# Kernel optimization log

Hardware: AMD Instinct MI355X
Metric: run time of the kernel (lower is better)

## Reference

```python
import jax, jax.numpy as jnp
import numpy as np
import math

EPS = 1e-5

def _ln(x, g, b):
    m = jnp.mean(x, axis=-1, keepdims=True)
    v = jnp.var(x, axis=-1, keepdims=True)
    return (x - m) * jax.lax.rsqrt(v + EPS) * g + b

def _rn_layer(x, W, g, b, A, Bb, Rw):
    # x: (B,S,in) -> (B,S,out). W: (out,in), A: (out,basis), Bb: (basis,out)
    S = x.shape[1]
    basis_dim = Bb.shape[0]
    n = _ln(x @ W.T, g, b)                      # (B,S,out)
    j = jnp.arange(S) % basis_dim               # (S,)
    Bv = Bb[j]                                  # (S,out)
    scal = jnp.einsum('bsd,sd->bs', n, Bv)      # (B,S)
    Av = A[:, j].T                              # (S,out)
    nf = scal[..., None] * Av                   # (B,S,out)
    res = x if Rw is None else x @ Rw.T
    return nf + res

def _ts_layer(x, M, g, b, P, Rw):
    # x: (B,S,in) -> (B,S,out). M: (out,in), P: (out,out,G)
    S = x.shape[1]
    D, _, G = P.shape
    t = _ln(x @ M.T, g, b)                      # (B,S,out)
    k = jnp.arange(S, dtype=jnp.float32)
    periods = (jnp.arange(D, dtype=jnp.float32)[:, None, None] * (D * G)
               + jnp.arange(D, dtype=jnp.float32)[None, :, None] * G
               + jnp.arange(G, dtype=jnp.float32)[None, None, :] + 2.0)  # (D,D,G)
    phi = jnp.cos(2.0 * math.pi * k[:, None, None, None] / periods)       # (S,D,D,G)
    # Nk[b,s,i] = sum_{j,g} P[i,j,g] * t[b,s,j] * phi[s,i,j,g]
    Wp = jnp.einsum('ijg,sijg->sij', P, phi)    # (S,D,D)
    Nk = jnp.einsum('sij,bsj->bsi', Wp, t)      # (B,S,D)
    return Nk + x @ Rw.T

def setup_inputs() -> dict:
    key = jax.random.key(0)
    ks = jax.random.split(key, 16)
    B, S = 2, 2048
    d0, d1, d2 = 512, 64, 512        # input_dim, ts out, final out
    bas1, G, bas3 = 64, 8, 64
    u = lambda k, sh, a: jax.random.uniform(k, sh, jnp.float32, -a, a)
    inp = {
        'x':  jax.random.normal(ks[0], (B, S, d0), jnp.float32),
        # Layer 1: RN 512->512 (in==out -> no residual proj)
        'W1': u(ks[1], (d0, d0), 0.1),
        'g1': jnp.ones((d0,), jnp.float32),
        'b1': jnp.zeros((d0,), jnp.float32),
        'A1': u(ks[2], (d0, bas1), 0.1),
        'B1': u(ks[3], (bas1, d0), 0.1),
        # Layer 2: TS 512->64
        'M2': u(ks[4], (d1, d0), 0.5),
        'g2': jnp.ones((d1,), jnp.float32),
        'b2': jnp.zeros((d1,), jnp.float32),
        'P2': u(ks[5], (d1, d1, G), 0.1),
        'R2': u(ks[6], (d1, d0), 0.1),
        # Layer 3: RN 64->512
        'W3': u(ks[7], (d2, d1), 0.1),
        'g3': jnp.ones((d2,), jnp.float32),
        'b3': jnp.zeros((d2,), jnp.float32),
        'A3': u(ks[8], (d2, bas3), 0.1),
        'B3': u(ks[9], (bas3, d2), 0.1),
        'R3': u(ks[10], (d2, d1), 0.1),
    }
    return inp

def reference(x, W1, g1, b1, A1, B1, M2, g2, b2, P2, R2, W3, g3, b3, A3, B3, R3):
    h = _rn_layer(x, W1, g1, b1, A1, B1, None)   # (B,S,512), identity residual
    h = _ts_layer(h, M2, g2, b2, P2, R2)         # (B,S,64)
    h = _rn_layer(h, W3, g3, b3, A3, B3, R3)     # (B,S,512)
    return h
```

## Files before the change

### kernel.cpp

```cpp
#include <hip/hip_runtime.h>
#include <math.h>

#define SEQ  2048
#define ROWS 4096
#define D0   512
#define D1   64
#define C2S  524288

typedef short bf8 __attribute__((ext_vector_type(8)));
typedef float f4  __attribute__((ext_vector_type(4)));

__device__ __forceinline__ unsigned short f2bf(float f) {
    unsigned u = __float_as_uint(f);
    return (unsigned short)((u + 0x7fffu + ((u >> 16) & 1u)) >> 16);
}
__device__ __forceinline__ float bf2f(unsigned short u) {
    return __uint_as_float((unsigned)u << 16);
}
__device__ __forceinline__ void hilo(float f, unsigned short& h, unsigned short& l) {
    h = f2bf(f);
    float fh = bf2f(h);
    l = f2bf(f - fh);
}
__device__ __forceinline__ void cv4h(unsigned short* dh, int idx, float4 v) {
    ushort4 hv;
    hv.x = f2bf(v.x); hv.y = f2bf(v.y); hv.z = f2bf(v.z); hv.w = f2bf(v.w);
    *(ushort4*)(dh + idx) = hv;
}

__device__ __forceinline__ void async16(const void* g, void* l) {
    __builtin_amdgcn_global_load_lds(
        (const __attribute__((address_space(1))) unsigned int*)g,
        (__attribute__((address_space(3))) unsigned int*)l, 16, 0, 0);
}

__global__ __launch_bounds__(256) void convk(
        const float* __restrict__ x,  const float* __restrict__ W1,
        const float* __restrict__ M2, const float* __restrict__ R2,
        const float* __restrict__ W3, const float* __restrict__ R3,
        const float* __restrict__ A1, const float* __restrict__ A3,
        unsigned short* __restrict__ xh, unsigned short* __restrict__ xl,
        unsigned short* __restrict__ W1h,
        unsigned short* __restrict__ C2h,
        unsigned short* __restrict__ C3h,
        float* __restrict__ A3T,
        float* __restrict__ G2y, float* __restrict__ G2r) {
    __shared__ float sh[4][64];
    int c = blockIdx.x, tid = threadIdx.x;
    if (c < 1024) {
        int base = c * 2048 + tid * 4;
        float4 v0 = *(const float4*)(x + base);
        float4 v1 = *(const float4*)(x + base + 1024);
        ushort4 h, l;
        hilo(v0.x, h.x, l.x); hilo(v0.y, h.y, l.y);
        hilo(v0.z, h.z, l.z); hilo(v0.w, h.w, l.w);
        *(ushort4*)(xh + base) = h; *(ushort4*)(xl + base) = l;
        hilo(v1.x, h.x, l.x); hilo(v1.y, h.y, l.y);
        hilo(v1.z, h.z, l.z); hilo(v1.w, h.w, l.w);
        *(ushort4*)(xh + base + 1024) = h; *(ushort4*)(xl + base + 1024) = l;
    } else if (c < 1216) {
        const float* src; unsigned short* dh; int off;
        if      (c < 1152) { src = W1; dh = W1h;         off = c - 1024; }
        else if (c < 1168) { src = M2; dh = C2h;         off = c - 1152; }
        else if (c < 1184) { src = R2; dh = C2h + 32768; off = c - 1168; }
        else if (c < 1200) { src = W3; dh = C3h;         off = c - 1184; }
        else               { src = R3; dh = C3h + 32768; off = c - 1200; }
        int base = off * 2048 + tid * 4;
        cv4h(dh, base,        *(const float4*)(src + base));
        cv4h(dh, base + 1024, *(const float4*)(src + base + 1024));
    } else if (c < 1344) {
        int gid = (c - 1216) * 256 + tid;
        int i = gid >> 6, j = gid & 63;
        A3T[j * 512 + i] = A3[gid];
    } else {
        int jrow = (c - 1344) & 63;
        const float* wv = (c < 1408) ? (M2 + jrow * 512) : (R2 + jrow * 512);
        float* G = (c < 1408) ? G2y : G2r;
        int jm = tid & 63, q = tid >> 6;
        const float* ap = A1 + (q * 128) * 64 + jm;
        const float* wp = wv + q * 128;
        float acc = 0.f;
        for (int cc = 0; cc < 128; ++cc)
            acc = fmaf(ap[cc * 64], wp[cc], acc);
        sh[q][jm] = acc;
        __syncthreads();
        if (tid < 64)
            G[tid * 64 + jrow] = (sh[0][tid] + sh[1][tid]) + (sh[2][tid] + sh[3][tid]);
    }
}

template<int AMODE, int OM>
__global__ __launch_bounds__(256, 4) void gemm128t(
        const unsigned short* __restrict__ Ah, const unsigned short* __restrict__ Al,
        const unsigned short* __restrict__ Wh,
        float* __restrict__ Cf, unsigned short* __restrict__ Cb,
        int N, int K, int Ks) {
    __shared__ __align__(16) unsigned short aH[8192];
    __shared__ __align__(16) unsigned short aL[AMODE ? 8192 : 16];
    __shared__ __align__(16) unsigned short wHs[4096];
    const int tid = threadIdx.x;
    const int wv  = tid >> 6;
    const int ln  = tid & 63;
    const int lm  = ln & 15;
    const int lq  = ln >> 4;
    const int bm  = blockIdx.y * 128;
    const int bn  = blockIdx.x * 64;
    const int k0  = blockIdx.z * Ks;
    const bool alo = (AMODE == 1) || (AMODE == 2 && bn >= 512);

    f4 acc[2][4] = {};

    for (int kt = 0; kt < Ks; kt += 64) {
        const int kg = k0 + kt;
        __syncthreads();
#pragma unroll
        for (int i = 0; i < 4; ++i) {
            int slot = i * 256 + wv * 64 + ln;
            int row  = slot >> 3;
            int ch   = (slot & 7) ^ (row & 7);
            size_t go = (size_t)(bm + row) * K + kg + ch * 8;
            async16(Ah + go, aH + slot * 8);
            if (alo) async16(Al + go, aL + slot * 8);
        }
#pragma unroll
        for (int i = 0; i < 2; ++i) {
            int slot = i * 256 + wv * 64 + ln;
            int row  = slot >> 3;
            int ch   = (slot & 7) ^ (row & 7);
            size_t go = (size_t)(bn + row) * K + kg + ch * 8;
            async16(Wh + go, wHs + slot * 8);
        }
        __syncthreads();

#pragma unroll
        for (int kk = 0; kk < 2; ++kk) {
            const int ck = kk * 4 + lq;
            bf8 a_h[2], a_l[2], b_h[4];
#pragma unroll
            for (int t = 0; t < 2; ++t) {
                int r = wv * 32 + t * 16 + lm;
                a_h[t] = *(const bf8*)(aH + r * 64 + ((ck ^ (r & 7)) * 8));
                if (alo)
                    a_l[t] = *(const bf8*)(aL + r * 64 + ((ck ^ (r & 7)) * 8));
            }
#pragma unroll
            for (int u = 0; u < 4; ++u) {
                int rb = u * 16 + lm;
                b_h[u] = *(const bf8*)(wHs + rb * 64 + ((ck ^ (rb & 7)) * 8));
            }
#pragma unroll
            for (int t = 0; t < 2; ++t)
#pragma unroll
                for (int u = 0; u < 4; ++u) {
                    acc[t][u] = __builtin_amdgcn_mfma_f32_16x16x32_bf16(a_h[t], b_h[u], acc[t][u], 0, 0, 0);
                    if (alo)
                        acc[t][u] = __builtin_amdgcn_mfma_f32_16x16x32_bf16(a_l[t], b_h[u], acc[t][u], 0, 0, 0);
                }
        }
    }

#pragma unroll
    for (int t = 0; t < 2; ++t)
#pragma unroll
        for (int u = 0; u < 4; ++u) {
            int row = bm + wv * 32 + t * 16 + lq * 4;
            int col = bn + u * 16 + lm;
#pragma unroll
            for (int r = 0; r < 4; ++r) {
                float v = acc[t][u][r];
                if constexpr (OM == 2) {
                    if (col < 512) Cb[(size_t)(row + r) * 512 + col] = f2bf(v);
                    else           Cf[(size_t)(row + r) * 512 + col - 512] = v;
                } else {
                    if (col < 512)
                        Cb[(size_t)blockIdx.z * ROWS * 512 + (size_t)(row + r) * 512 + col] = f2bf(v);
                    else
                        Cf[(size_t)blockIdx.z * ROWS * 128 + (size_t)(row + r) * 128 + (col - 512)] = v;
                }
            }
        }
}

__global__ __launch_bounds__(256) void ptk(
        const unsigned short* __restrict__ C1b,
        const float* __restrict__ C2,
        const float* __restrict__ B1,
        const float* __restrict__ g1, const float* __restrict__ b1,
        const float* __restrict__ g2, const float* __restrict__ b2,
        const float* __restrict__ G2y, const float* __restrict__ G2r,
        float* __restrict__ t, float* __restrict__ rsum) {
    const int row = blockIdx.x * 4 + (threadIdx.x >> 6);
    const int l = threadIdx.x & 63;
    const int c = l * 8;
    const int jm = row & 63;
    const size_t rb0 = (size_t)row * 512 + c;
    ushort4 ua = *(const ushort4*)(C1b + rb0);
    ushort4 ub = *(const ushort4*)(C1b + rb0 + 4);
    ushort4 va = *(const ushort4*)(C1b + (size_t)ROWS * 512 + rb0);
    ushort4 vb = *(const ushort4*)(C1b + (size_t)ROWS * 512 + rb0 + 4);
    float y[8];
    y[0] = bf2f(ua.x) + bf2f(va.x); y[1] = bf2f(ua.y) + bf2f(va.y);
    y[2] = bf2f(ua.z) + bf2f(va.z); y[3] = bf2f(ua.w) + bf2f(va.w);
    y[4] = bf2f(ub.x) + bf2f(vb.x); y[5] = bf2f(ub.y) + bf2f(vb.y);
    y[6] = bf2f(ub.z) + bf2f(vb.z); y[7] = bf2f(ub.w) + bf2f(vb.w);
    float4 B0  = *(const float4*)(B1 + jm * 512 + c);
    float4 B1q = *(const float4*)(B1 + jm * 512 + c + 4);
    float4 gg0 = *(const float4*)(g1 + c), gg1 = *(const float4*)(g1 + c + 4);
    float4 bb0 = *(const float4*)(b1 + c), bb1 = *(const float4*)(b1 + c + 4);
    float Bv[8] = {B0.x, B0.y, B0.z, B0.w, B1q.x, B1q.y, B1q.z, B1q.w};
    float gv[8] = {gg0.x, gg0.y, gg0.z, gg0.w, gg1.x, gg1.y, gg1.z, gg1.w};
    float bv[8] = {bb0.x, bb0.y, bb0.z, bb0.w, bb1.x, bb1.y, bb1.z, bb1.w};
    float sum = 0.f, ssq = 0.f, S1 = 0.f, SU = 0.f, SBB = 0.f;
#pragma unroll
    for (int i = 0; i < 8; ++i) {
        float u = gv[i] * Bv[i];
        sum += y[i];
        ssq = fmaf(y[i], y[i], ssq);
        S1  = fmaf(y[i], u, S1);
        SU  += u;
        SBB = fmaf(bv[i], Bv[i], SBB);
    }
#pragma unroll
    for (int m = 1; m < 64; m <<= 1) {
        sum += __shfl_xor(sum, m, 64);
        ssq += __shfl_xor(ssq, m, 64);
        S1  += __shfl_xor(S1, m, 64);
        SU  += __shfl_xor(SU, m, 64);
        SBB += __shfl_xor(SBB, m, 64);
    }
    float mean = sum * (1.0f / 512.0f);
    float var  = ssq * (1.0f / 512.0f) - mean * mean;
    float rstd = rsqrtf(var + 1e-5f);
    float p = rstd * (S1 - mean * SU) + SBB;

    const size_t rb = (size_t)row * 128;
    float z  = C2[rb + l]      + C2[C2S + rb + l];
    float zr = C2[rb + 64 + l] + C2[C2S + rb + 64 + l];
    float v  = z  + p * G2y[jm * 64 + l];
    float rv = zr + p * G2r[jm * 64 + l];
    float s2 = v, q2 = v * v;
#pragma unroll
    for (int m = 1; m < 64; m <<= 1) {
        s2 += __shfl_xor(s2, m, 64);
        q2 += __shfl_xor(q2, m, 64);
    }
    float mean2 = s2 * (1.0f / 64.0f);
    float var2  = q2 * (1.0f / 64.0f) - mean2 * mean2;
    float rstd2 = rsqrtf(var2 + 1e-5f);
    t[row * 64 + l]    = (v - mean2) * rstd2 * g2[l] + b2[l];
    rsum[row * 64 + l] = rv;
}

__global__ __launch_bounds__(256) void lnrn(
        const unsigned short* __restrict__ Yb0,
        const float* __restrict__ RES,
        const float* __restrict__ g, const float* __restrict__ be,
        const float* __restrict__ Bb, const float* __restrict__ AaT,
        float* __restrict__ outf) {
    const int row = blockIdx.x * 4 + (threadIdx.x >> 6);
    const int l = threadIdx.x & 63;
    const int c = l * 8;
    ushort4 ua = *(const ushort4*)(Yb0 + (size_t)row * D0 + c);
    ushort4 ub = *(const ushort4*)(Yb0 + (size_t)row * D0 + c + 4);
    float4 y0, y1;
    y0.x = bf2f(ua.x); y0.y = bf2f(ua.y); y0.z = bf2f(ua.z); y0.w = bf2f(ua.w);
    y1.x = bf2f(ub.x); y1.y = bf2f(ub.y); y1.z = bf2f(ub.z); y1.w = bf2f(ub.w);
    float sum = y0.x + y0.y + y0.z + y0.w + y1.x + y1.y + y1.z + y1.w;
    float ssq = y0.x*y0.x + y0.y*y0.y + y0.z*y0.z + y0.w*y0.w
              + y1.x*y1.x + y1.y*y1.y + y1.z*y1.z + y1.w*y1.w;
#pragma unroll
    for (int m = 1; m < 64; m <<= 1) {
        sum += __shfl_xor(sum, m, 64);
        ssq += __shfl_xor(ssq, m, 64);
    }
    float mean = sum * (1.0f / 512.0f);
    float var  = ssq * (1.0f / 512.0f) - mean * mean;
    float rstd = rsqrtf(var + 1e-5f);
    float4 g0 = *(const float4*)(g + c),  g1v = *(const float4*)(g + c + 4);
    float4 e0 = *(const float4*)(be + c), e1  = *(const float4*)(be + c + 4);
    float4 n0, n1;
    n0.x = (y0.x - mean) * rstd * g0.x  + e0.x;
    n0.y = (y0.y - mean) * rstd * g0.y  + e0.y;
    n0.z = (y0.z - mean) * rstd * g0.z  + e0.z;
    n0.w = (y0.w - mean) * rstd * g0.w  + e0.w;
    n1.x = (y1.x - mean) * rstd * g1v.x + e1.x;
    n1.y = (y1.y - mean) * rstd * g1v.y + e1.y;
    n1.z = (y1.z - mean) * rstd * g1v.z + e1.z;
    n1.w = (y1.w - mean) * rstd * g1v.w + e1.w;
    const int jm = row & 63;
    const float* bb = Bb + jm * D0 + c;
    float4 b0 = *(const float4*)bb, b1v = *(const float4*)(bb + 4);
    float p = n0.x*b0.x + n0.y*b0.y + n0.z*b0.z + n0.w*b0.w
            + n1.x*b1v.x + n1.y*b1v.y + n1.z*b1v.z + n1.w*b1v.w;
#pragma unroll
    for (int m = 1; m < 64; m <<= 1) p += __shfl_xor(p, m, 64);
    const float* av = AaT + jm * D0 + c;
    float4 a0 = *(const float4*)av, a1 = *(const float4*)(av + 4);
    const float* rs = RES + (size_t)row * D0 + c;
    float4 r0 = *(const float4*)rs, r1 = *(const float4*)(rs + 4);
    float4 v0, v1;
    v0.x = p*a0.x + r0.x; v0.y = p*a0.y + r0.y; v0.z = p*a0.z + r0.z; v0.w = p*a0.w + r0.w;
    v1.x = p*a1.x + r1.x; v1.y = p*a1.y + r1.y; v1.z = p*a1.z + r1.z; v1.w = p*a1.w + r1.w;
    *(float4*)(outf + (size_t)row * D0 + c)     = v0;
    *(float4*)(outf + (size_t)row * D0 + c + 4) = v1;
}

__global__ __launch_bounds__(256) void tsk2(
        const float* __restrict__ t, const float* __restrict__ rsum,
        const float* __restrict__ P,
        unsigned short* __restrict__ Hh, unsigned short* __restrict__ Hl) {
    const int bid = blockIdx.x;
    const int i   = bid >> 3;
    const int sg  = bid & 7;
    const int w   = threadIdx.x >> 6;
    const int ln  = threadIdx.x & 63;
    const int s0  = sg * 256 + w * 64;
    const int idx = i * 64 + ln;
    const float* pp = P + idx * 8;
    const float sf0 = (float)s0;

    float k2c[8], ca[8], cb[8];
#pragma unroll
    for (int g = 0; g < 8; ++g) {
        float pf   = (float)(idx * 8 + g + 2);
        float invp = __builtin_amdgcn_rcpf(pf);
        k2c[g] = 2.0f * __builtin_amdgcn_cosf(invp);
        float q0 = floorf(sf0 * invp);
        float r0 = fmaf(-q0, pf, sf0);
        float f0 = r0 * invp; f0 -= floorf(f0);
        float c0 = __builtin_amdgcn_cosf(f0);
        float sf1 = sf0 + 1.0f;
        float q1 = floorf(sf1 * invp);
        float r1 = fmaf(-q1, pf, sf1);
        float f1 = r1 * invp; f1 -= floorf(f1);
        float c1 = __builtin_amdgcn_cosf(f1);
        float Pv = pp[g];
        ca[g] = Pv * c0;
        cb[g] = Pv * c1;
    }

    const int tb = s0 * 64 + ln;
    float t0c = t[tb], t1c = t[131072 + tb];
    float res0 = 0.f, res1 = 0.f;

    for (int st = 0; st < 64; st += 2) {
        float t0n  = t[tb + (st + 1) * 64];
        float t1n  = t[131072 + tb + (st + 1) * 64];
        float ws = ((ca[0] + ca[1]) + (ca[2] + ca[3]))
                 + ((ca[4] + ca[5]) + (ca[6] + ca[7]));
#pragma unroll
        for (int g = 0; g < 8; ++g) ca[g] = fmaf(k2c[g], cb[g], -ca[g]);
        float v0 = ws * t0c, v1 = ws * t1c;
#pragma unroll
        for (int m = 1; m < 64; m <<= 1) {
            v0 += __shfl_xor(v0, m, 64);
            v1 += __shfl_xor(v1, m, 64);
        }
        res0 = (ln == st) ? v0 : res0;
        res1 = (ln == st) ? v1 : res1;
        float t0n2 = t[tb + (st + 2) * 64];
        float t1n2 = t[131072 + tb + (st + 2) * 64];
        float ws2 = ((cb[0] + cb[1]) + (cb[2] + cb[3]))
                  + ((cb[4] + cb[5]) + (cb[6] + cb[7]));
#pragma unroll
        for (int g = 0; g < 8; ++g) cb[g] = fmaf(k2c[g], ca[g], -cb[g]);
        float v0b = ws2 * t0n, v1b = ws2 * t1n;
#pragma unroll
        for (int m = 1; m < 64; m <<= 1) {
            v0b += __shfl_xor(v0b, m, 64);
            v1b += __shfl_xor(v1b, m, 64);
        }
        res0 = (ln == st + 1) ? v0b : res0;
        res1 = (ln == st + 1) ? v1b : res1;
        t0c = t0n2; t1c = t1n2;
    }

    const int s = s0 + ln;
    {
        float v = res0 + rsum[(size_t)s * 64 + i];
        unsigned short h, l; hilo(v, h, l);
        Hh[(size_t)s * 64 + i] = h; Hl[(size_t)s * 64 + i] = l;
        float v1e = res1 + rsum[(size_t)(SEQ + s) * 64 + i];
        hilo(v1e, h, l);
        Hh[(size_t)(SEQ + s) * 64 + i] = h; Hl[(size_t)(SEQ + s) * 64 + i] = l;
    }
}

extern "C" void kernel_launch(void* const* d_in, const int* in_sizes, int n_in,
                              void* d_out, int out_size, void* d_ws, size_t ws_size,
                              hipStream_t stream) {
    (void)in_sizes; (void)n_in; (void)out_size; (void)ws_size;
    const float* x  = (const float*)d_in[0];
    const float* W1 = (const float*)d_in[1];
    const float* g1 = (const float*)d_in[2];
    const float* b1 = (const float*)d_in[3];
    const float* A1 = (const float*)d_in[4];
    const float* B1 = (const float*)d_in[5];
    const float* M2 = (const float*)d_in[6];
    const float* g2 = (const float*)d_in[7];
    const float* b2 = (const float*)d_in[8];
    const float* P2 = (const float*)d_in[9];
    const float* R2 = (const float*)d_in[10];
    const float* W3 = (const float*)d_in[11];
    const float* g3 = (const float*)d_in[12];
    const float* b3 = (const float*)d_in[13];
    const float* A3 = (const float*)d_in[14];
    const float* B3 = (const float*)d_in[15];
    const float* R3 = (const float*)d_in[16];

    float* ws = (float*)d_ws;
    float* C2   = ws;
    float* C3r  = ws + 2097152;
    float* t    = ws + 4194304;
    float* rsum = ws + 4456448;
    float* G2y  = ws + 4718592;
    float* G2r  = ws + 4722688;
    float* A3T  = ws + 4751360;
    unsigned short* us = (unsigned short*)(ws + 4784128);
    unsigned short* xh   = us;
    unsigned short* xl   = us + 2097152;
    unsigned short* W1h  = us + 6291456;
    unsigned short* Wc2h = us + 6553600;
    unsigned short* Wc3h = us + 6619136;
    unsigned short* h2h  = us + 6684672;
    unsigned short* h2l  = us + 6946816;
    unsigned short* C1b  = us + 7208960;
    unsigned short* C3n  = us + 11403264;

    dim3 blk(256);

    convk<<<1472, blk, 0, stream>>>(x, W1, M2, R2, W3, R3, A1, A3,
                                    xh, xl, W1h, Wc2h, Wc3h, A3T, G2y, G2r);

    gemm128t<2, 3><<<dim3(10, 32, 2), blk, 0, stream>>>(
        xh, xl, W1h, C2, C1b, 640, 512, 256);

    ptk<<<1024, blk, 0, stream>>>(C1b, C2, B1, g1, b1, g2, b2, G2y, G2r, t, rsum);

    tsk2<<<512, blk, 0, stream>>>(t, rsum, P2, h2h, h2l);

    gemm128t<1, 2><<<dim3(16, 32, 1), blk, 0, stream>>>(
        h2h, h2l, Wc3h, C3r, C3n, 1024, 64, 64);

    lnrn<<<1024, blk, 0, stream>>>(C3n, C3r, g3, b3, B3, A3T, (float*)d_out);
}
```

Before: 146.7 us.

## Fuse layer-3 GEMM with LayerNorm/basis epilogue into single kernel

Replaces the final GEMM launch and the separate lnrn kernel with one kernel. Each block computes a 16-row by 1024-column tile (512 main, 512 residual) into shared memory, then applies LayerNorm and the basis projection in the epilogue. The scalar is computed algebraically from S1, SU and SBB sums, so the normalized vector is never materialized. This removes the round trip of the bf16 and fp32 intermediates through global memory plus one launch, but gives only 256 blocks with heavy shared memory use (about 100KB), which limits occupancy.

```diff
diff --git a/kernel.cpp b/kernel.cpp
--- a/kernel.cpp
+++ b/kernel.cpp
@@ -168,15 +168,10 @@
 #pragma unroll
             for (int r = 0; r < 4; ++r) {
                 float v = acc[t][u][r];
-                if constexpr (OM == 2) {
-                    if (col < 512) Cb[(size_t)(row + r) * 512 + col] = f2bf(v);
-                    else           Cf[(size_t)(row + r) * 512 + col - 512] = v;
-                } else {
-                    if (col < 512)
-                        Cb[(size_t)blockIdx.z * ROWS * 512 + (size_t)(row + r) * 512 + col] = f2bf(v);
-                    else
-                        Cf[(size_t)blockIdx.z * ROWS * 128 + (size_t)(row + r) * 128 + (col - 512)] = v;
-                }
+                if (col < 512)
+                    Cb[(size_t)blockIdx.z * ROWS * 512 + (size_t)(row + r) * 512 + col] = f2bf(v);
+                else
+                    Cf[(size_t)blockIdx.z * ROWS * 128 + (size_t)(row + r) * 128 + (col - 512)] = v;
             }
         }
 }
@@ -251,60 +246,6 @@
     rsum[row * 64 + l] = rv;
 }
 
-__global__ __launch_bounds__(256) void lnrn(
-        const unsigned short* __restrict__ Yb0,
-        const float* __restrict__ RES,
-        const float* __restrict__ g, const float* __restrict__ be,
-        const float* __restrict__ Bb, const float* __restrict__ AaT,
-        float* __restrict__ outf) {
-    const int row = blockIdx.x * 4 + (threadIdx.x >> 6);
-    const int l = threadIdx.x & 63;
-    const int c = l * 8;
-    ushort4 ua = *(const ushort4*)(Yb0 + (size_t)row * D0 + c);
-    ushort4 ub = *(const ushort4*)(Yb0 + (size_t)row * D0 + c + 4);
-    float4 y0, y1;
-    y0.x = bf2f(ua.x); y0.y = bf2f(ua.y); y0.z = bf2f(ua.z); y0.w = bf2f(ua.w);
-    y1.x = bf2f(ub.x); y1.y = bf2f(ub.y); y1.z = bf2f(ub.z); y1.w = bf2f(ub.w);
-    float sum = y0.x + y0.y + y0.z + y0.w + y1.x + y1.y + y1.z + y1.w;
-    float ssq = y0.x*y0.x + y0.y*y0.y + y0.z*y0.z + y0.w*y0.w
-              + y1.x*y1.x + y1.y*y1.y + y1.z*y1.z + y1.w*y1.w;
-#pragma unroll
-    for (int m = 1; m < 64; m <<= 1) {
-        sum += __shfl_xor(sum, m, 64);
-        ssq += __shfl_xor(ssq, m, 64);
-    }
-    float mean = sum * (1.0f / 512.0f);
-    float var  = ssq * (1.0f / 512.0f) - mean * mean;
-    float rstd = rsqrtf(var + 1e-5f);
-    float4 g0 = *(const float4*)(g + c),  g1v = *(const float4*)(g + c + 4);
-    float4 e0 = *(const float4*)(be + c), e1  = *(const float4*)(be + c + 4);
-    float4 n0, n1;
-    n0.x = (y0.x - mean) * rstd * g0.x  + e0.x;
-    n0.y = (y0.y - mean) * rstd * g0.y  + e0.y;
-    n0.z = (y0.z - mean) * rstd * g0.z  + e0.z;
-    n0.w = (y0.w - mean) * rstd * g0.w  + e0.w;
-    n1.x = (y1.x - mean) * rstd * g1v.x + e1.x;
-    n1.y = (y1.y - mean) * rstd * g1v.y + e1.y;
-    n1.z = (y1.z - mean) * rstd * g1v.z + e1.z;
-    n1.w = (y1.w - mean) * rstd * g1v.w + e1.w;
-    const int jm = row & 63;
-    const float* bb = Bb + jm * D0 + c;
-    float4 b0 = *(const float4*)bb, b1v = *(const float4*)(bb + 4);
-    float p = n0.x*b0.x + n0.y*b0.y + n0.z*b0.z + n0.w*b0.w
-            + n1.x*b1v.x + n1.y*b1v.y + n1.z*b1v.z + n1.w*b1v.w;
-#pragma unroll
-    for (int m = 1; m < 64; m <<= 1) p += __shfl_xor(p, m, 64);
-    const float* av = AaT + jm * D0 + c;
-    float4 a0 = *(const float4*)av, a1 = *(const float4*)(av + 4);
-    const float* rs = RES + (size_t)row * D0 + c;
-    float4 r0 = *(const float4*)rs, r1 = *(const float4*)(rs + 4);
-    float4 v0, v1;
-    v0.x = p*a0.x + r0.x; v0.y = p*a0.y + r0.y; v0.z = p*a0.z + r0.z; v0.w = p*a0.w + r0.w;
-    v1.x = p*a1.x + r1.x; v1.y = p*a1.y + r1.y; v1.z = p*a1.z + r1.z; v1.w = p*a1.w + r1.w;
-    *(float4*)(outf + (size_t)row * D0 + c)     = v0;
-    *(float4*)(outf + (size_t)row * D0 + c + 4) = v1;
-}
-
 __global__ __launch_bounds__(256) void tsk2(
         const float* __restrict__ t, const float* __restrict__ rsum,
         const float* __restrict__ P,
@@ -383,6 +324,120 @@
         float v1e = res1 + rsum[(size_t)(SEQ + s) * 64 + i];
         hilo(v1e, h, l);
         Hh[(size_t)(SEQ + s) * 64 + i] = h; Hl[(size_t)(SEQ + s) * 64 + i] = l;
+    }
+}
+
+__global__ __launch_bounds__(256) void g3ln(
+        const unsigned short* __restrict__ Hh, const unsigned short* __restrict__ Hl,
+        const unsigned short* __restrict__ Wc3h,
+        const float* __restrict__ g3, const float* __restrict__ b3,
+        const float* __restrict__ B3, const float* __restrict__ A3T,
+        float* __restrict__ outf) {
+    __shared__ __align__(16) unsigned short aH[1024];
+    __shared__ __align__(16) unsigned short aL[1024];
+    __shared__ __align__(16) unsigned short wS[16384];
+    __shared__ float cS[16 * 1024];
+    const int tid = threadIdx.x;
+    const int wv  = tid >> 6;
+    const int ln  = tid & 63;
+    const int lm  = ln & 15;
+    const int lq  = ln >> 4;
+    const int r0  = blockIdx.x * 16;
+
+    {
+        int slot = (wv & 1) * 64 + ln;
+        int row  = slot >> 3;
+        int ch   = (slot & 7) ^ (row & 7);
+        size_t go = (size_t)(r0 + row) * 64 + ch * 8;
+        if (wv < 2) async16(Hh + go, aH + slot * 8);
+        else        async16(Hl + go, aL + slot * 8);
+    }
+
+    bf8 ah[2], al[2];
+    for (int q = 0; q < 4; ++q) {
+#pragma unroll
+        for (int i = 0; i < 8; ++i) {
+            int slot = i * 256 + tid;
+            int lr   = slot >> 3;
+            int ch   = (slot & 7) ^ (lr & 7);
+            int grow = (lr >> 6) * 256 + q * 64 + (lr & 63);
+            size_t go = (size_t)grow * 64 + ch * 8;
+            async16(Wc3h + go, wS + slot * 8);
+        }
+        __syncthreads();
+        if (q == 0) {
+#pragma unroll
+            for (int kk = 0; kk < 2; ++kk) {
+                int ck = kk * 4 + lq;
+                ah[kk] = *(const bf8*)(aH + lm * 64 + ((ck ^ (lm & 7)) * 8));
+                al[kk] = *(const bf8*)(aL + lm * 64 + ((ck ^ (lm & 7)) * 8));
+            }
+        }
+        f4 acc[4] = {};
+#pragma unroll
+        for (int kk = 0; kk < 2; ++kk) {
+            int ck = kk * 4 + lq;
+            bf8 bh[4];
+#pragma unroll
+            for (int u = 0; u < 4; ++u) {
+                int lr = wv * 64 + u * 16 + lm;
+                bh[u] = *(const bf8*)(wS + lr * 64 + ((ck ^ (lr & 7)) * 8));
+            }
+#pragma unroll
+            for (int u = 0; u < 4; ++u) {
+                acc[u] = __builtin_amdgcn_mfma_f32_16x16x32_bf16(ah[kk], bh[u], acc[u], 0, 0, 0);
+                acc[u] = __builtin_amdgcn_mfma_f32_16x16x32_bf16(al[kk], bh[u], acc[u], 0, 0, 0);
+            }
+        }
+#pragma unroll
+        for (int u = 0; u < 4; ++u) {
+            int col = wv * 256 + q * 64 + u * 16 + lm;
+#pragma unroll
+            for (int r = 0; r < 4; ++r)
+                cS[(lq * 4 + r) * 1024 + col] = acc[u][r];
+        }
+        __syncthreads();
+    }
+
+    for (int rr = 0; rr < 4; ++rr) {
+        int row  = wv * 4 + rr;
+        int grow = r0 + row;
+        int jm   = grow & 63;
+        const float* Bp = B3  + jm * 512;
+        const float* Ap = A3T + jm * 512;
+        float sum = 0.f, ssq = 0.f, S1 = 0.f, SU = 0.f, SBB = 0.f;
+#pragma unroll
+        for (int k = 0; k < 8; ++k) {
+            int col = ln + k * 64;
+            float y  = cS[row * 1024 + col];
+            float Bv = Bp[col];
+            float gv = g3[col];
+            float bv = b3[col];
+            float u = gv * Bv;
+            sum += y;
+            ssq = fmaf(y, y, ssq);
+            S1  = fmaf(y, u, S1);
+            SU  += u;
+            SBB = fmaf(bv, Bv, SBB);
+        }
+#pragma unroll
+        for (int m = 1; m < 64; m <<= 1) {
+            sum += __shfl_xor(sum, m, 64);
+            ssq += __shfl_xor(ssq, m, 64);
+            S1  += __shfl_xor(S1, m, 64);
+            SU  += __shfl_xor(SU, m, 64);
+            SBB += __shfl_xor(SBB, m, 64);
+        }
+        float mean = sum * (1.0f / 512.0f);
+        float var  = ssq * (1.0f / 512.0f) - mean * mean;
+        float rstd = rsqrtf(var + 1e-5f);
+        float p = rstd * (S1 - mean * SU) + SBB;
+#pragma unroll
+        for (int k = 0; k < 8; ++k) {
+            int col = ln + k * 64;
+            float res = cS[row * 1024 + 512 + col];
+            outf[(size_t)grow * 512 + col] = fmaf(p, Ap[col], res);
+        }
     }
 }
 
@@ -410,7 +465,6 @@
 
     float* ws = (float*)d_ws;
     float* C2   = ws;
-    float* C3r  = ws + 2097152;
     float* t    = ws + 4194304;
     float* rsum = ws + 4456448;
     float* G2y  = ws + 4718592;
@@ -425,7 +479,6 @@
     unsigned short* h2h  = us + 6684672;
     unsigned short* h2l  = us + 6946816;
     unsigned short* C1b  = us + 7208960;
-    unsigned short* C3n  = us + 11403264;
 
     dim3 blk(256);
 
@@ -439,8 +492,5 @@
 
     tsk2<<<512, blk, 0, stream>>>(t, rsum, P2, h2h, h2l);
 
-    gemm128t<1, 2><<<dim3(16, 32, 1), blk, 0, stream>>>(
-        h2h, h2l, Wc3h, C3r, C3n, 1024, 64, 64);
-
-    lnrn<<<1024, blk, 0, stream>>>(C3n, C3r, g3, b3, B3, A3T, (float*)d_out);
-}
+    g3ln<<<256, blk, 0, stream>>>(h2h, h2l, Wc3h, g3, b3, B3, A3T, (float*)d_out);
+}
```

Measured after the change: 143.7 us. -2.1%, faster.
